# Performance work log

Measured on AMD Instinct MI355X. Metric: run time of the kernel, lower is better.

Reference implementation:

```python
import jax, jax.numpy as jnp
import numpy as np

DIM = 384
HEADS = 6
HEAD_DIM = DIM // HEADS
MLP_DIM = int(DIM * 4.0)
EPS = 1e-5


def layer_norm(x, g, b):
    mu = jnp.mean(x, axis=-1, keepdims=True)
    var = jnp.mean(jnp.square(x - mu), axis=-1, keepdims=True)
    return (x - mu) * jax.lax.rsqrt(var + EPS) * g + b


def setup_inputs() -> dict:
    key = jax.random.key(0)
    ks = jax.random.split(key, 12)
    s = 0.02
    return {
        "x": jax.random.normal(ks[0], (8, 2048, DIM), dtype=jnp.float32),
        "ln1_g": jnp.ones((DIM,), jnp.float32),
        "ln1_b": jnp.zeros((DIM,), jnp.float32),
        "qkv_w": jax.random.normal(ks[1], (DIM, 3 * DIM), jnp.float32) * s,
        "qkv_b": jnp.zeros((3 * DIM,), jnp.float32),
        "proj_w": jax.random.normal(ks[2], (DIM, DIM), jnp.float32) * s,
        "proj_b": jnp.zeros((DIM,), jnp.float32),
        "ln2_g": jnp.ones((DIM,), jnp.float32),
        "ln2_b": jnp.zeros((DIM,), jnp.float32),
        "fc1_w": jax.random.normal(ks[3], (DIM, MLP_DIM), jnp.float32) * s,
        "fc1_b": jnp.zeros((MLP_DIM,), jnp.float32),
        "fc2_w": jax.random.normal(ks[4], (MLP_DIM, DIM), jnp.float32) * s,
        "fc2_b": jnp.zeros((DIM,), jnp.float32),
    }


def reference(x, ln1_g, ln1_b, qkv_w, qkv_b, proj_w, proj_b,
              ln2_g, ln2_b, fc1_w, fc1_b, fc2_w, fc2_b):
    B, N, C = x.shape
    # --- attention ---
    h = layer_norm(x, ln1_g, ln1_b)
    qkv = h @ qkv_w + qkv_b  # [B,N,3C]
    qkv = qkv.reshape(B, N, 3, HEADS, HEAD_DIM)
    q, k, v = jnp.moveaxis(qkv, 2, 0)  # each [B,N,H,D]
    scale = HEAD_DIM ** -0.5
    attn = jnp.einsum('bnhd,bmhd->bhnm', q, k) * scale  # [B,H,N,N]
    attn = jax.nn.softmax(attn, axis=-1)
    o = jnp.einsum('bhnm,bmhd->bnhd', attn, v).reshape(B, N, C)
    x = x + o @ proj_w + proj_b
    # --- mlp ---
    h = layer_norm(x, ln2_g, ln2_b)
    h = jax.nn.gelu(h @ fc1_w + fc1_b, approximate=False)
    x = x + h @ fc2_w + fc2_b
    return x
```

## Files before the change

kernel.cpp:

```cpp
#include <hip/hip_runtime.h>
#include <hip/hip_bf16.h>

#define DIM   384
#define SEQ   2048
#define BATCH 8
#define NHEAD 6
#define HD    64
#define MLPD  1536
#define MTOT  (BATCH*SEQ)

typedef __attribute__((ext_vector_type(8))) short bf16x8;
typedef __attribute__((ext_vector_type(4))) float f32x4;

static __device__ __forceinline__ float bf2f(unsigned short u){
    union { float f; unsigned int i; } v; v.i = ((unsigned int)u) << 16; return v.f;
}
static __device__ __forceinline__ unsigned short f2bf(float f){
    union { float f; unsigned int i; } v; v.f = f;
    unsigned int r = v.i + 0x7fffu + ((v.i >> 16) & 1u);
    return (unsigned short)(r >> 16);
}
static __device__ __forceinline__ unsigned int asu(float f){
    union { float f; unsigned int i; } v; v.f = f; return v.i;
}
static __device__ __forceinline__ void gload_lds16(const unsigned short* g, unsigned short* l){
    __builtin_amdgcn_global_load_lds(
        (__attribute__((address_space(1))) void*)(g),
        (__attribute__((address_space(3))) void*)(l), 16, 0, 0);
}
static __device__ __forceinline__ void barx(){
    asm volatile("" ::: "memory");
    __builtin_amdgcn_s_barrier();
    asm volatile("" ::: "memory");
}
#define WAITVM(N) asm volatile("s_waitcnt vmcnt(" #N ")" ::: "memory")

__global__ __launch_bounds__(256) void wt_all_kernel(
    const float* __restrict__ qkv_w, const float* __restrict__ proj_w,
    const float* __restrict__ fc1_w, const float* __restrict__ fc2_w,
    unsigned short* __restrict__ o_qkv, unsigned short* __restrict__ o_prj,
    unsigned short* __restrict__ o_fc1, unsigned short* __restrict__ o_fc2)
{
    __shared__ float tile[64][68];
    int bid = blockIdx.x;
    const float* W; unsigned short* Wt; int K, N, tk, tn;
    if (bid < 108)      { W = qkv_w; Wt = o_qkv; K = 384;  N = 1152; tk = bid/18;        tn = bid%18; }
    else if (bid < 144) { W = proj_w; Wt = o_prj; K = 384;  N = 384;  tk = (bid-108)/6;  tn = (bid-108)%6; }
    else if (bid < 288) { W = fc1_w; Wt = o_fc1; K = 384;  N = 1536; tk = (bid-144)/24; tn = (bid-144)%24; }
    else                { W = fc2_w; Wt = o_fc2; K = 1536; N = 384;  tk = (bid-288)/6;  tn = (bid-288)%6; }
    int t = threadIdx.x;
    int lr = t >> 4, lc = (t & 15) * 4;
#pragma unroll
    for (int p = 0; p < 4; p++){
        float4 v = *(const float4*)(W + (size_t)(tk*64 + p*16 + lr) * N + tn*64 + lc);
        *(float4*)&tile[p*16 + lr][lc] = v;
    }
    __syncthreads();
    int n = t >> 2, k0 = (t & 3) * 16;
    unsigned int w[8];
#pragma unroll
    for (int i = 0; i < 8; i++)
        w[i] = (unsigned int)f2bf(tile[k0 + 2*i][n]) | ((unsigned int)f2bf(tile[k0 + 2*i + 1][n]) << 16);
    unsigned short* dst = Wt + (size_t)(tn*64 + n) * K + tk*64 + k0;
    *(uint4*)(dst)     = make_uint4(w[0], w[1], w[2], w[3]);
    *(uint4*)(dst + 8) = make_uint4(w[4], w[5], w[6], w[7]);
}

__global__ __launch_bounds__(256) void ln_kernel(const float* __restrict__ x,
                                                 const float* __restrict__ g,
                                                 const float* __restrict__ b,
                                                 unsigned short* __restrict__ out){
    int row  = blockIdx.x * 4 + (threadIdx.x >> 6);
    int lane = threadIdx.x & 63;
    const float* xr = x + (size_t)row * DIM;
    float v[6];
#pragma unroll
    for (int p = 0; p < 3; p++){
        float2 t = *(const float2*)(xr + lane * 2 + p * 128);
        v[2*p] = t.x; v[2*p+1] = t.y;
    }
    float s = 0.f, sq = 0.f;
#pragma unroll
    for (int i = 0; i < 6; i++){ s += v[i]; sq += v[i] * v[i]; }
#pragma unroll
    for (int off = 1; off < 64; off <<= 1){
        s  += __shfl_xor(s, off);
        sq += __shfl_xor(sq, off);
    }
    float mu   = s * (1.0f / DIM);
    float var  = sq * (1.0f / DIM) - mu * mu;
    float rstd = rsqrtf(var + 1e-5f);
    unsigned short* orow = out + (size_t)row * DIM;
#pragma unroll
    for (int p = 0; p < 3; p++){
        int c = lane * 2 + p * 128;
        float h0 = (v[2*p]   - mu) * rstd * g[c]   + b[c];
        float h1 = (v[2*p+1] - mu) * rstd * g[c+1] + b[c+1];
        unsigned int pk = (unsigned int)f2bf(h0) | ((unsigned int)f2bf(h1) << 16);
        *(unsigned int*)(orow + c) = pk;
    }
}

template<int OFF>
static __device__ __forceinline__ void gemm_tile(const unsigned short* smem,
                                                 int wid, int quad, int l15,
                                                 f32x4 acc[2][8])
{
#pragma unroll
    for (int kk = 0; kk < 2; kk++){
        bf16x8 af[2], bf[8];
#pragma unroll
        for (int i = 0; i < 2; i++){
            int r = wid*32 + i*16 + l15;
            af[i] = *(const bf16x8*)&smem[OFF + r * 64 + (((kk*4 + quad) ^ (l15 & 7)) * 8)];
        }
#pragma unroll
        for (int j = 0; j < 8; j++){
            int r = j*16 + l15;
            bf[j] = *(const bf16x8*)&smem[OFF + 4096 + r * 64 + (((kk*4 + quad) ^ (l15 & 7)) * 8)];
        }
#pragma unroll
        for (int i = 0; i < 2; i++)
#pragma unroll
            for (int j = 0; j < 8; j++)
                acc[i][j] = __builtin_amdgcn_mfma_f32_16x16x32_bf16(af[i], bf[j], acc[i][j], 0, 0, 0);
    }
}

template<int EPI, int K>
__global__ __launch_bounds__(128, 3) void gemm_kernel(
    const unsigned short* __restrict__ A, const unsigned short* __restrict__ Bt,
    const float* __restrict__ bias, int N,
    const float* __restrict__ resid, float* __restrict__ outf,
    unsigned short* __restrict__ outb,
    unsigned short* __restrict__ qb, unsigned short* __restrict__ kb2,
    unsigned short* __restrict__ vb)
{
    __shared__ __align__(16) unsigned short smem[2 * 12288];
    int t = threadIdx.x;
    int wid = t >> 6, lane = t & 63, quad = lane >> 4, l15 = lane & 15;
    int row0 = blockIdx.y * 64, col0 = blockIdx.x * 128;
    int sr = lane >> 3, sc = lane & 7;
    int scl = (sc ^ sr) * 8;

    const unsigned short* A0 = A  + (size_t)(row0 + wid*32 + sr) * K + scl;
    const unsigned short* B0 = Bt + (size_t)(col0 + wid*64 + sr) * K + scl;
    int kc = 0;

#define GSTAGE(LOFF) do { \
    _Pragma("unroll") \
    for (int jj = 0; jj < 4; jj++) \
        gload_lds16(A0 + jj*8*K + kc, &smem[(LOFF) + (wid*32 + jj*8) * 64]); \
    _Pragma("unroll") \
    for (int jj = 0; jj < 8; jj++) \
        gload_lds16(B0 + jj*8*K + kc, &smem[(LOFF) + 4096 + (wid*64 + jj*8) * 64]); \
    kc += 64; } while(0)

    f32x4 acc[2][8];
    f32x4 zz = {0.f, 0.f, 0.f, 0.f};
#pragma unroll
    for (int i = 0; i < 2; i++)
#pragma unroll
        for (int j = 0; j < 8; j++) acc[i][j] = zz;

    GSTAGE(0);
    constexpr int PAIRS = K / 128;
    for (int p = 0; p < PAIRS - 1; p++){
        GSTAGE(12288);
        WAITVM(12);
        barx();
        gemm_tile<0>(smem, wid, quad, l15, acc);
        barx();
        GSTAGE(0);
        WAITVM(12);
        barx();
        gemm_tile<12288>(smem, wid, quad, l15, acc);
        barx();
    }
    GSTAGE(12288);
    WAITVM(12);
    barx();
    gemm_tile<0>(smem, wid, quad, l15, acc);
    barx();
    WAITVM(0);
    barx();
    gemm_tile<12288>(smem, wid, quad, l15, acc);
#undef GSTAGE

    if (EPI == 0 && col0 >= 768){
        __syncthreads();
        unsigned short* T = smem;
#pragma unroll
        for (int i = 0; i < 2; i++)
#pragma unroll
            for (int j = 0; j < 8; j++){
                int gcl = j*16 + l15;
                float bia = bias[col0 + gcl];
                int nsl0 = wid*32 + i*16 + quad*4;
#pragma unroll
                for (int r = 0; r < 4; r++)
                    T[gcl * 72 + nsl0 + r] = f2bf(acc[i][j][r] + bia);
            }
        __syncthreads();
        int rem = (col0 - 768) + t;
        int head = rem >> 6, d = rem & 63;
        int bidx = row0 >> 11, ns0 = row0 & 2047;
        unsigned short* dst = vb + ((size_t)((bidx * NHEAD + head) * 64 + d)) * SEQ + ns0;
        const unsigned short* src = T + t * 72;
#pragma unroll
        for (int m = 0; m < 8; m++)
            *(uint4*)(dst + m*8) = *(const uint4*)(src + m*8);
        return;
    }

#pragma unroll
    for (int i = 0; i < 2; i++){
#pragma unroll
        for (int j = 0; j < 8; j++){
            int gr0 = row0 + wid*32 + i*16 + quad*4;
            int gc  = col0 + j*16 + l15;
            float bia = bias[gc];
#pragma unroll
            for (int r = 0; r < 4; r++){
                int gr = gr0 + r;
                float val = acc[i][j][r] + bia;
                if (EPI == 1){
                    outf[(size_t)gr * N + gc] = resid[(size_t)gr * N + gc] + val;
                } else if (EPI == 2){
                    float u = val * (1.0f + 0.044715f * val * val);
                    float e = __builtin_amdgcn_exp2f(u * 2.3025851f);
                    outb[(size_t)gr * N + gc] = f2bf(val * e / (e + 1.0f));
                } else {
                    int trip = gc / 384, remq = gc - trip * 384;
                    int head = remq >> 6, d = remq & 63;
                    int bidx = gr >> 11, ns = gr & 2047;
                    size_t off = ((size_t)(bidx * NHEAD + head) * SEQ + ns) * 64 + d;
                    unsigned short* dstp = (trip == 0) ? qb : kb2;
                    dstp[off] = f2bf(val);
                }
            }
        }
    }
}

template<int LOFF>
static __device__ __forceinline__ void attn_tile(
    const bf16x8 (&qf)[2][2], const bf16x8& ones,
    const unsigned short* const (&kf_ptr)[4][2],
    const unsigned short* const (&vf_ptr)[2][4],
    const unsigned short* const (&pf_ptr)[2][2],
    uint2* const (&pw_ptr)[2][4],
    f32x4 (&sacc)[2], f32x4 (&oacc)[2][4])
{
    const f32x4 zz = {0.f, 0.f, 0.f, 0.f};
    f32x4 st[2][4];
#pragma unroll
    for (int n = 0; n < 4; n++){
        bf16x8 kf0 = *(const bf16x8*)(kf_ptr[n][0] + LOFF);
        bf16x8 kf1 = *(const bf16x8*)(kf_ptr[n][1] + LOFF);
#pragma unroll
        for (int h = 0; h < 2; h++){
            f32x4 z = __builtin_amdgcn_mfma_f32_16x16x32_bf16(kf0, qf[h][0], zz, 0, 0, 0);
            st[h][n] = __builtin_amdgcn_mfma_f32_16x16x32_bf16(kf1, qf[h][1], z, 0, 0, 0);
        }
    }
#pragma unroll
    for (int h = 0; h < 2; h++){
#pragma unroll
        for (int n = 0; n < 4; n++){
            float p0 = __builtin_amdgcn_exp2f(st[h][n][0]);
            float p1 = __builtin_amdgcn_exp2f(st[h][n][1]);
            float p2 = __builtin_amdgcn_exp2f(st[h][n][2]);
            float p3 = __builtin_amdgcn_exp2f(st[h][n][3]);
            unsigned int w0 = __builtin_amdgcn_perm(asu(p1), asu(p0), 0x07060302u);
            unsigned int w1 = __builtin_amdgcn_perm(asu(p3), asu(p2), 0x07060302u);
            *pw_ptr[h][n] = make_uint2(w0, w1);
        }
    }
    asm volatile("s_waitcnt lgkmcnt(0)" ::: "memory");
#pragma unroll
    for (int c = 0; c < 2; c++){
        bf16x8 pf[2];
#pragma unroll
        for (int h = 0; h < 2; h++)
            pf[h] = *(const bf16x8*)pf_ptr[c][h];
        sacc[0] = __builtin_amdgcn_mfma_f32_16x16x32_bf16(ones, pf[0], sacc[0], 0, 0, 0);
        sacc[1] = __builtin_amdgcn_mfma_f32_16x16x32_bf16(ones, pf[1], sacc[1], 0, 0, 0);
#pragma unroll
        for (int dn = 0; dn < 4; dn++){
            bf16x8 vf = *(const bf16x8*)(vf_ptr[c][dn] + LOFF);
            oacc[0][dn] = __builtin_amdgcn_mfma_f32_16x16x32_bf16(vf, pf[0], oacc[0][dn], 0, 0, 0);
            oacc[1][dn] = __builtin_amdgcn_mfma_f32_16x16x32_bf16(vf, pf[1], oacc[1][dn], 0, 0, 0);
        }
    }
}

__global__ __launch_bounds__(128, 3) void attn_kernel(const unsigned short* __restrict__ Q,
                                                      const unsigned short* __restrict__ Kb,
                                                      const unsigned short* __restrict__ Vt,
                                                      unsigned short* __restrict__ O){
    __shared__ __align__(16) unsigned short smem[2*4096 + 2*4096 + 2*2048];

    int bh = blockIdx.y, qt = blockIdx.x;
    int t = threadIdx.x, wid = t >> 6, lane = t & 63, quad = lane >> 4, l15 = lane & 15;
    int l7 = l15 & 7;
    int q0 = qt * 64 + wid * 32;
    const unsigned short* Qp = Q  + (size_t)bh * SEQ * 64;
    const unsigned short* Kp = Kb + (size_t)bh * SEQ * 64;
    const unsigned short* Vp = Vt + (size_t)bh * 64 * SEQ;
    int sr = lane >> 3, sc = lane & 7;
    int scl = (sc ^ sr) * 8;

    const float QSCALE = 0.125f * 1.44269504f;
    bf16x8 qf[2][2];
#pragma unroll
    for (int h = 0; h < 2; h++){
#pragma unroll
        for (int c = 0; c < 2; c++){
            union { uint4 u; unsigned short s[8]; } cv;
            cv.u = *(const uint4*)(Qp + (size_t)(q0 + h*16 + l15) * 64 + c * 32 + quad * 8);
            bf16x8 f;
#pragma unroll
            for (int j = 0; j < 8; j++) f[j] = (short)f2bf(bf2f(cv.s[j]) * QSCALE);
            qf[h][c] = f;
        }
    }

    bf16x8 ones;
#pragma unroll
    for (int j = 0; j < 8; j++) ones[j] = (short)0x3F80;

    f32x4 oacc[2][4], sacc[2];
    f32x4 zz = {0.f, 0.f, 0.f, 0.f};
#pragma unroll
    for (int h = 0; h < 2; h++){
        sacc[h] = zz;
#pragma unroll
        for (int dn = 0; dn < 4; dn++) oacc[h][dn] = zz;
    }
    unsigned short* P = &smem[16384 + wid * 2048];

    const unsigned short* kf_ptr[4][2];
#pragma unroll
    for (int n = 0; n < 4; n++){
        int kv = n * 16 + l15;
        kf_ptr[n][0] = &smem[kv * 64 + ((quad       ^ (kv & 7)) * 8)];
        kf_ptr[n][1] = &smem[kv * 64 + (((4 + quad) ^ (kv & 7)) * 8)];
    }
    const unsigned short* vf_ptr[2][4];
#pragma unroll
    for (int c = 0; c < 2; c++)
#pragma unroll
        for (int dn = 0; dn < 4; dn++){
            int d = dn * 16 + l15;
            vf_ptr[c][dn] = &smem[8192 + d * 64 + (((c*4 + quad) ^ (d & 7)) * 8)];
        }
    const unsigned short* pf_ptr[2][2];
#pragma unroll
    for (int c = 0; c < 2; c++)
#pragma unroll
        for (int h = 0; h < 2; h++)
            pf_ptr[c][h] = P + (h*16 + l15) * 64 + (((c*4 + quad) ^ l7) * 8);
    uint2* pw_ptr[2][4];
#pragma unroll
    for (int h = 0; h < 2; h++)
#pragma unroll
        for (int n = 0; n < 4; n++){
            int qloc = h * 16 + l15;
            int chunk = n * 2 + (quad >> 1);
            pw_ptr[h][n] = (uint2*)(P + qloc * 64 + ((chunk ^ l7) * 8) + (quad & 1) * 4);
        }
    const unsigned short* kstage[4];
    const unsigned short* vstage[4];
    unsigned short* klds[4];
    unsigned short* vlds[4];
#pragma unroll
    for (int jj = 0; jj < 4; jj++){
        int rb = wid * 32 + jj * 8;
        kstage[jj] = Kp + (size_t)(rb + sr) * 64 + scl;
        vstage[jj] = Vp + (size_t)(rb + sr) * SEQ + scl;
        klds[jj] = &smem[rb * 64];
        vlds[jj] = &smem[8192 + rb * 64];
    }

#define AISSUE(BOFF) do { \
    _Pragma("unroll") \
    for (int jj = 0; jj < 4; jj++){ \
        gload_lds16(kstage[jj], klds[jj] + (BOFF)); \
        gload_lds16(vstage[jj], vlds[jj] + (BOFF)); \
        kstage[jj] += 64 * 64; \
        vstage[jj] += 64; \
    } } while(0)

    AISSUE(0);
    for (int p = 0; p < SEQ/128 - 1; p++){
        AISSUE(4096);
        WAITVM(8);
        barx();
        attn_tile<0>(qf, ones, kf_ptr, vf_ptr, pf_ptr, pw_ptr, sacc, oacc);
        barx();
        AISSUE(0);
        WAITVM(8);
        barx();
        attn_tile<4096>(qf, ones, kf_ptr, vf_ptr, pf_ptr, pw_ptr, sacc, oacc);
        barx();
    }
    AISSUE(4096);
    WAITVM(8);
    barx();
    attn_tile<0>(qf, ones, kf_ptr, vf_ptr, pf_ptr, pw_ptr, sacc, oacc);
    barx();
    WAITVM(0);
    barx();
    attn_tile<4096>(qf, ones, kf_ptr, vf_ptr, pf_ptr, pw_ptr, sacc, oacc);
#undef AISSUE

    int b = bh / NHEAD, hh = bh - b * NHEAD;
#pragma unroll
    for (int h = 0; h < 2; h++){
        float rd = 1.0f / sacc[h][0];
        size_t row = (size_t)(b * SEQ + q0 + h*16 + l15);
#pragma unroll
        for (int dn = 0; dn < 4; dn++){
            float v0 = oacc[h][dn][0] * rd, v1 = oacc[h][dn][1] * rd;
            float v2 = oacc[h][dn][2] * rd, v3 = oacc[h][dn][3] * rd;
            unsigned int w0 = (unsigned int)f2bf(v0) | ((unsigned int)f2bf(v1) << 16);
            unsigned int w1 = (unsigned int)f2bf(v2) | ((unsigned int)f2bf(v3) << 16);
            *(uint2*)(O + row * DIM + hh * 64 + dn * 16 + quad * 4) = make_uint2(w0, w1);
        }
    }
}

extern "C" void kernel_launch(void* const* d_in, const int* in_sizes, int n_in,
                              void* d_out, int out_size, void* d_ws, size_t ws_size,
                              hipStream_t stream){
    const float* x      = (const float*)d_in[0];
    const float* ln1_g  = (const float*)d_in[1];
    const float* ln1_b  = (const float*)d_in[2];
    const float* qkv_w  = (const float*)d_in[3];
    const float* qkv_b  = (const float*)d_in[4];
    const float* proj_w = (const float*)d_in[5];
    const float* proj_b = (const float*)d_in[6];
    const float* ln2_g  = (const float*)d_in[7];
    const float* ln2_b  = (const float*)d_in[8];
    const float* fc1_w  = (const float*)d_in[9];
    const float* fc1_b  = (const float*)d_in[10];
    const float* fc2_w  = (const float*)d_in[11];
    const float* fc2_b  = (const float*)d_in[12];
    float* out = (float*)d_out;

    char* p = (char*)d_ws;
    auto take = [&](size_t n){ char* r = p; p += (n + 255) & ~(size_t)255; return r; };
    unsigned short* wt_qkv = (unsigned short*)take((size_t)1152 * 384 * 2);
    unsigned short* wt_prj = (unsigned short*)take((size_t)384 * 384 * 2);
    unsigned short* wt_fc1 = (unsigned short*)take((size_t)1536 * 384 * 2);
    unsigned short* wt_fc2 = (unsigned short*)take((size_t)384 * 1536 * 2);
    unsigned short* rbig   = (unsigned short*)take((size_t)MTOT * 4 * DIM * 2);
    unsigned short* h2     = (unsigned short*)take((size_t)MTOT * DIM * 2);
    float*          x1     = (float*)take((size_t)MTOT * DIM * 4);

    unsigned short* h1     = rbig;
    unsigned short* qb     = rbig + (size_t)MTOT * DIM;
    unsigned short* kb     = qb   + (size_t)MTOT * DIM;
    unsigned short* vb     = kb   + (size_t)MTOT * DIM;
    unsigned short* attn_o = rbig;
    unsigned short* hm     = rbig;

    wt_all_kernel<<<dim3(432), 256, 0, stream>>>(qkv_w, proj_w, fc1_w, fc2_w,
                                                 wt_qkv, wt_prj, wt_fc1, wt_fc2);
    ln_kernel<<<dim3(MTOT/4), 256, 0, stream>>>(x, ln1_g, ln1_b, h1);
    gemm_kernel<0,384><<<dim3(9, 256), 128, 0, stream>>>(h1, wt_qkv, qkv_b, 1152,
                                                     nullptr, nullptr, nullptr, qb, kb, vb);
    attn_kernel<<<dim3(SEQ/64, BATCH*NHEAD), 128, 0, stream>>>(qb, kb, vb, attn_o);
    gemm_kernel<1,384><<<dim3(3, 256), 128, 0, stream>>>(attn_o, wt_prj, proj_b, 384,
                                                     x, x1, nullptr, nullptr, nullptr, nullptr);
    ln_kernel<<<dim3(MTOT/4), 256, 0, stream>>>(x1, ln2_g, ln2_b, h2);
    gemm_kernel<2,384><<<dim3(12, 256), 128, 0, stream>>>(h2, wt_fc1, fc1_b, 1536,
                                                      nullptr, nullptr, hm, nullptr, nullptr, nullptr);
    gemm_kernel<1,1536><<<dim3(3, 256), 128, 0, stream>>>(hm, wt_fc2, fc2_b, 384,
                                                     x1, out, nullptr, nullptr, nullptr, nullptr);
}
```

Measured before the change: 322.8 us.

## Reshape GEMM tiles to 128x64 with 4 waves and double attention block rows

GEMM blocks now use 256 threads (4 waves) computing a 128x64 output tile instead of 2 waves on 64x128, so each wave holds 2x4 accumulators rather than 2x8. Load staging, LDS offsets, the V-transpose epilogue and the Q/K scatter epilogue are rewritten to match, and the Q/K path now resolves the head once per block. The attention kernel also moves to 4 waves per block covering 128 queries, sharing each K/V tile across more waves. The aim is higher occupancy and lower register pressure, at the cost of less B-operand reuse per wave and more blocks in flight.

```diff
diff --git a/kernel.cpp b/kernel.cpp
--- a/kernel.cpp
+++ b/kernel.cpp
@@ -104,31 +104,31 @@
 template<int OFF>
 static __device__ __forceinline__ void gemm_tile(const unsigned short* smem,
                                                  int wid, int quad, int l15,
-                                                 f32x4 acc[2][8])
+                                                 f32x4 (&acc)[2][4])
 {
 #pragma unroll
     for (int kk = 0; kk < 2; kk++){
-        bf16x8 af[2], bf[8];
+        bf16x8 af[2], bf[4];
 #pragma unroll
         for (int i = 0; i < 2; i++){
             int r = wid*32 + i*16 + l15;
             af[i] = *(const bf16x8*)&smem[OFF + r * 64 + (((kk*4 + quad) ^ (l15 & 7)) * 8)];
         }
 #pragma unroll
-        for (int j = 0; j < 8; j++){
+        for (int j = 0; j < 4; j++){
             int r = j*16 + l15;
-            bf[j] = *(const bf16x8*)&smem[OFF + 4096 + r * 64 + (((kk*4 + quad) ^ (l15 & 7)) * 8)];
+            bf[j] = *(const bf16x8*)&smem[OFF + 8192 + r * 64 + (((kk*4 + quad) ^ (l15 & 7)) * 8)];
         }
 #pragma unroll
         for (int i = 0; i < 2; i++)
 #pragma unroll
-            for (int j = 0; j < 8; j++)
+            for (int j = 0; j < 4; j++)
                 acc[i][j] = __builtin_amdgcn_mfma_f32_16x16x32_bf16(af[i], bf[j], acc[i][j], 0, 0, 0);
     }
 }
 
 template<int EPI, int K>
-__global__ __launch_bounds__(128, 3) void gemm_kernel(
+__global__ __launch_bounds__(256, 3) void gemm_kernel(
     const unsigned short* __restrict__ A, const unsigned short* __restrict__ Bt,
     const float* __restrict__ bias, int N,
     const float* __restrict__ resid, float* __restrict__ outf,
@@ -139,12 +139,12 @@
     __shared__ __align__(16) unsigned short smem[2 * 12288];
     int t = threadIdx.x;
     int wid = t >> 6, lane = t & 63, quad = lane >> 4, l15 = lane & 15;
-    int row0 = blockIdx.y * 64, col0 = blockIdx.x * 128;
+    int row0 = blockIdx.y * 128, col0 = blockIdx.x * 64;
     int sr = lane >> 3, sc = lane & 7;
     int scl = (sc ^ sr) * 8;
 
     const unsigned short* A0 = A  + (size_t)(row0 + wid*32 + sr) * K + scl;
-    const unsigned short* B0 = Bt + (size_t)(col0 + wid*64 + sr) * K + scl;
+    const unsigned short* B0 = Bt + (size_t)(col0 + wid*16 + sr) * K + scl;
     int kc = 0;
 
 #define GSTAGE(LOFF) do { \
@@ -152,33 +152,33 @@
     for (int jj = 0; jj < 4; jj++) \
         gload_lds16(A0 + jj*8*K + kc, &smem[(LOFF) + (wid*32 + jj*8) * 64]); \
     _Pragma("unroll") \
-    for (int jj = 0; jj < 8; jj++) \
-        gload_lds16(B0 + jj*8*K + kc, &smem[(LOFF) + 4096 + (wid*64 + jj*8) * 64]); \
+    for (int jj = 0; jj < 2; jj++) \
+        gload_lds16(B0 + jj*8*K + kc, &smem[(LOFF) + 8192 + (wid*16 + jj*8) * 64]); \
     kc += 64; } while(0)
 
-    f32x4 acc[2][8];
+    f32x4 acc[2][4];
     f32x4 zz = {0.f, 0.f, 0.f, 0.f};
 #pragma unroll
     for (int i = 0; i < 2; i++)
 #pragma unroll
-        for (int j = 0; j < 8; j++) acc[i][j] = zz;
+        for (int j = 0; j < 4; j++) acc[i][j] = zz;
 
     GSTAGE(0);
     constexpr int PAIRS = K / 128;
     for (int p = 0; p < PAIRS - 1; p++){
         GSTAGE(12288);
-        WAITVM(12);
+        WAITVM(6);
         barx();
         gemm_tile<0>(smem, wid, quad, l15, acc);
         barx();
         GSTAGE(0);
-        WAITVM(12);
+        WAITVM(6);
         barx();
         gemm_tile<12288>(smem, wid, quad, l15, acc);
         barx();
     }
     GSTAGE(12288);
-    WAITVM(12);
+    WAITVM(6);
     barx();
     gemm_tile<0>(smem, wid, quad, l15, acc);
     barx();
@@ -193,30 +193,52 @@
 #pragma unroll
         for (int i = 0; i < 2; i++)
 #pragma unroll
-            for (int j = 0; j < 8; j++){
+            for (int j = 0; j < 4; j++){
                 int gcl = j*16 + l15;
                 float bia = bias[col0 + gcl];
                 int nsl0 = wid*32 + i*16 + quad*4;
 #pragma unroll
                 for (int r = 0; r < 4; r++)
-                    T[gcl * 72 + nsl0 + r] = f2bf(acc[i][j][r] + bia);
+                    T[gcl * 136 + nsl0 + r] = f2bf(acc[i][j][r] + bia);
             }
         __syncthreads();
-        int rem = (col0 - 768) + t;
-        int head = rem >> 6, d = rem & 63;
+        int head = (col0 - 768) >> 6;
         int bidx = row0 >> 11, ns0 = row0 & 2047;
-        unsigned short* dst = vb + ((size_t)((bidx * NHEAD + head) * 64 + d)) * SEQ + ns0;
-        const unsigned short* src = T + t * 72;
-#pragma unroll
-        for (int m = 0; m < 8; m++)
+        int d = t >> 2, qq = t & 3;
+        unsigned short* dst = vb + ((size_t)((bidx * NHEAD + head) * 64 + d)) * SEQ + ns0 + qq*32;
+        const unsigned short* src = T + d * 136 + qq * 32;
+#pragma unroll
+        for (int m = 0; m < 4; m++)
             *(uint4*)(dst + m*8) = *(const uint4*)(src + m*8);
         return;
     }
 
+    if (EPI == 0){
+        int trip = (col0 >= 384) ? 1 : 0;
+        int head = (col0 - trip*384) >> 6;
+        unsigned short* dstp = trip ? kb2 : qb;
+#pragma unroll
+        for (int i = 0; i < 2; i++)
+#pragma unroll
+            for (int j = 0; j < 4; j++){
+                int d = j*16 + l15;
+                float bia = bias[col0 + d];
+                int gr0 = row0 + wid*32 + i*16 + quad*4;
+#pragma unroll
+                for (int r = 0; r < 4; r++){
+                    int gr = gr0 + r;
+                    int bidx = gr >> 11, ns = gr & 2047;
+                    dstp[((size_t)(bidx * NHEAD + head) * SEQ + ns) * 64 + d] =
+                        f2bf(acc[i][j][r] + bia);
+                }
+            }
+        return;
+    }
+
 #pragma unroll
     for (int i = 0; i < 2; i++){
 #pragma unroll
-        for (int j = 0; j < 8; j++){
+        for (int j = 0; j < 4; j++){
             int gr0 = row0 + wid*32 + i*16 + quad*4;
             int gc  = col0 + j*16 + l15;
             float bia = bias[gc];
@@ -226,17 +248,10 @@
                 float val = acc[i][j][r] + bia;
                 if (EPI == 1){
                     outf[(size_t)gr * N + gc] = resid[(size_t)gr * N + gc] + val;
-                } else if (EPI == 2){
+                } else {
                     float u = val * (1.0f + 0.044715f * val * val);
                     float e = __builtin_amdgcn_exp2f(u * 2.3025851f);
                     outb[(size_t)gr * N + gc] = f2bf(val * e / (e + 1.0f));
-                } else {
-                    int trip = gc / 384, remq = gc - trip * 384;
-                    int head = remq >> 6, d = remq & 63;
-                    int bidx = gr >> 11, ns = gr & 2047;
-                    size_t off = ((size_t)(bidx * NHEAD + head) * SEQ + ns) * 64 + d;
-                    unsigned short* dstp = (trip == 0) ? qb : kb2;
-                    dstp[off] = f2bf(val);
                 }
             }
         }
@@ -295,16 +310,16 @@
     }
 }
 
-__global__ __launch_bounds__(128, 3) void attn_kernel(const unsigned short* __restrict__ Q,
+__global__ __launch_bounds__(256, 3) void attn_kernel(const unsigned short* __restrict__ Q,
                                                       const unsigned short* __restrict__ Kb,
                                                       const unsigned short* __restrict__ Vt,
                                                       unsigned short* __restrict__ O){
-    __shared__ __align__(16) unsigned short smem[2*4096 + 2*4096 + 2*2048];
+    __shared__ __align__(16) unsigned short smem[16384 + 4*2048];
 
     int bh = blockIdx.y, qt = blockIdx.x;
     int t = threadIdx.x, wid = t >> 6, lane = t & 63, quad = lane >> 4, l15 = lane & 15;
     int l7 = l15 & 7;
-    int q0 = qt * 64 + wid * 32;
+    int q0 = qt * 128 + wid * 32;
     const unsigned short* Qp = Q  + (size_t)bh * SEQ * 64;
     const unsigned short* Kp = Kb + (size_t)bh * SEQ * 64;
     const unsigned short* Vp = Vt + (size_t)bh * 64 * SEQ;
@@ -353,7 +368,7 @@
 #pragma unroll
         for (int dn = 0; dn < 4; dn++){
             int d = dn * 16 + l15;
-            vf_ptr[c][dn] = &smem[8192 + d * 64 + (((c*4 + quad) ^ (d & 7)) * 8)];
+            vf_ptr[c][dn] = &smem[4096 + d * 64 + (((c*4 + quad) ^ (d & 7)) * 8)];
         }
     const unsigned short* pf_ptr[2][2];
 #pragma unroll
@@ -370,22 +385,22 @@
             int chunk = n * 2 + (quad >> 1);
             pw_ptr[h][n] = (uint2*)(P + qloc * 64 + ((chunk ^ l7) * 8) + (quad & 1) * 4);
         }
-    const unsigned short* kstage[4];
-    const unsigned short* vstage[4];
-    unsigned short* klds[4];
-    unsigned short* vlds[4];
-#pragma unroll
-    for (int jj = 0; jj < 4; jj++){
-        int rb = wid * 32 + jj * 8;
+    const unsigned short* kstage[2];
+    const unsigned short* vstage[2];
+    unsigned short* klds[2];
+    unsigned short* vlds[2];
+#pragma unroll
+    for (int jj = 0; jj < 2; jj++){
+        int rb = wid * 16 + jj * 8;
         kstage[jj] = Kp + (size_t)(rb + sr) * 64 + scl;
         vstage[jj] = Vp + (size_t)(rb + sr) * SEQ + scl;
         klds[jj] = &smem[rb * 64];
-        vlds[jj] = &smem[8192 + rb * 64];
+        vlds[jj] = &smem[4096 + rb * 64];
     }
 
 #define AISSUE(BOFF) do { \
     _Pragma("unroll") \
-    for (int jj = 0; jj < 4; jj++){ \
+    for (int jj = 0; jj < 2; jj++){ \
         gload_lds16(kstage[jj], klds[jj] + (BOFF)); \
         gload_lds16(vstage[jj], vlds[jj] + (BOFF)); \
         kstage[jj] += 64 * 64; \
@@ -394,25 +409,25 @@
 
     AISSUE(0);
     for (int p = 0; p < SEQ/128 - 1; p++){
-        AISSUE(4096);
-        WAITVM(8);
+        AISSUE(8192);
+        WAITVM(4);
         barx();
         attn_tile<0>(qf, ones, kf_ptr, vf_ptr, pf_ptr, pw_ptr, sacc, oacc);
         barx();
         AISSUE(0);
-        WAITVM(8);
-        barx();
-        attn_tile<4096>(qf, ones, kf_ptr, vf_ptr, pf_ptr, pw_ptr, sacc, oacc);
-        barx();
-    }
-    AISSUE(4096);
-    WAITVM(8);
+        WAITVM(4);
+        barx();
+        attn_tile<8192>(qf, ones, kf_ptr, vf_ptr, pf_ptr, pw_ptr, sacc, oacc);
+        barx();
+    }
+    AISSUE(8192);
+    WAITVM(4);
     barx();
     attn_tile<0>(qf, ones, kf_ptr, vf_ptr, pf_ptr, pw_ptr, sacc, oacc);
     barx();
     WAITVM(0);
     barx();
-    attn_tile<4096>(qf, ones, kf_ptr, vf_ptr, pf_ptr, pw_ptr, sacc, oacc);
+    attn_tile<8192>(qf, ones, kf_ptr, vf_ptr, pf_ptr, pw_ptr, sacc, oacc);
 #undef AISSUE
 
     int b = bh / NHEAD, hh = bh - b * NHEAD;
@@ -469,14 +484,14 @@
     wt_all_kernel<<<dim3(432), 256, 0, stream>>>(qkv_w, proj_w, fc1_w, fc2_w,
                                                  wt_qkv, wt_prj, wt_fc1, wt_fc2);
     ln_kernel<<<dim3(MTOT/4), 256, 0, stream>>>(x, ln1_g, ln1_b, h1);
-    gemm_kernel<0,384><<<dim3(9, 256), 128, 0, stream>>>(h1, wt_qkv, qkv_b, 1152,
+    gemm_kernel<0,384><<<dim3(18, 128), 256, 0, stream>>>(h1, wt_qkv, qkv_b, 1152,
                                                      nullptr, nullptr, nullptr, qb, kb, vb);
-    attn_kernel<<<dim3(SEQ/64, BATCH*NHEAD), 128, 0, stream>>>(qb, kb, vb, attn_o);
-    gemm_kernel<1,384><<<dim3(3, 256), 128, 0, stream>>>(attn_o, wt_prj, proj_b, 384,
+    attn_kernel<<<dim3(SEQ/128, BATCH*NHEAD), 256, 0, stream>>>(qb, kb, vb, attn_o);
+    gemm_kernel<1,384><<<dim3(6, 128), 256, 0, stream>>>(attn_o, wt_prj, proj_b, 384,
                                                      x, x1, nullptr, nullptr, nullptr, nullptr);
     ln_kernel<<<dim3(MTOT/4), 256, 0, stream>>>(x1, ln2_g, ln2_b, h2);
-    gemm_kernel<2,384><<<dim3(12, 256), 128, 0, stream>>>(h2, wt_fc1, fc1_b, 1536,
+    gemm_kernel<2,384><<<dim3(24, 128), 256, 0, stream>>>(h2, wt_fc1, fc1_b, 1536,
                                                       nullptr, nullptr, hm, nullptr, nullptr, nullptr);
-    gemm_kernel<1,1536><<<dim3(3, 256), 128, 0, stream>>>(hm, wt_fc2, fc2_b, 384,
+    gemm_kernel<1,1536><<<dim3(6, 128), 256, 0, stream>>>(hm, wt_fc2, fc2_b, 384,
                                                      x1, out, nullptr, nullptr, nullptr, nullptr);
 }
```

Measured after the change: 305.4 us. 1.06x faster.
